# Kernel optimization log

Measured on AMD Instinct MI355X. Metric: run time of the kernel, lower is better.

## Reference

```python
import jax, jax.numpy as jnp
import numpy as np

N, E, F_IN, HID, EDIM = 20000, 320000, 16, 64, 1


def _add_self_loops(src, dst, eattr, n):
    # PyG add_self_loops with fill_value='mean': self-loop edge_attr = mean of
    # incoming edge_attr per destination node (0 if no incoming edges).
    deg = jax.ops.segment_sum(jnp.ones_like(eattr[:, 0]), dst, num_segments=n)
    mean_attr = jax.ops.segment_sum(eattr, dst, num_segments=n) / jnp.maximum(deg, 1.0)[:, None]
    loop = jnp.arange(n)
    return (jnp.concatenate([src, loop]), jnp.concatenate([dst, loop]),
            jnp.concatenate([eattr, mean_attr], axis=0))


def _gat_layer(x, src, dst, eattr, W, a_src, a_dst, We, a_e, b, heads, out_ch, n):
    # shared linear for src/dst (PyG GATConv with int in_channels)
    h = (x @ W).reshape(n, heads, out_ch)                      # [N,H,C]
    al_s = jnp.einsum('nhc,hc->nh', h, a_src)                  # [N,H]
    al_d = jnp.einsum('nhc,hc->nh', h, a_dst)
    ef = (eattr @ We).reshape(-1, heads, out_ch)               # [E,H,C]
    al_e = jnp.einsum('ehc,hc->eh', ef, a_e)                   # [E,H]
    alpha = jax.nn.leaky_relu(al_s[src] + al_d[dst] + al_e, 0.2)
    # segment softmax over destination node
    m = jax.ops.segment_max(alpha, dst, num_segments=n)
    m = jnp.where(jnp.isfinite(m), m, 0.0)
    ex = jnp.exp(alpha - m[dst])
    den = jax.ops.segment_sum(ex, dst, num_segments=n)
    coef = ex / (den[dst] + 1e-16)                             # [E,H]
    out = jax.ops.segment_sum(h[src] * coef[:, :, None], dst, num_segments=n)
    return out.reshape(n, heads * out_ch) + b


def setup_inputs() -> dict:
    key = jax.random.key(0)
    ks = jax.random.split(key, 24)
    s = 0.1
    inp = {
        'x': jax.random.normal(ks[0], (N, F_IN), jnp.float32),
        'edge_index': jax.random.randint(ks[1], (2, E), 0, N, jnp.int64),
        'edge_attr': jax.random.uniform(ks[2], (E, EDIM), jnp.float32),
        # layer 0: heads=4, in=16, out=64
        'W0': jax.random.normal(ks[3], (F_IN, 4 * HID), jnp.float32) * s,
        'as0': jax.random.normal(ks[4], (4, HID), jnp.float32) * s,
        'ad0': jax.random.normal(ks[5], (4, HID), jnp.float32) * s,
        'We0': jax.random.normal(ks[6], (EDIM, 4 * HID), jnp.float32) * s,
        'ae0': jax.random.normal(ks[7], (4, HID), jnp.float32) * s,
        'b0': jnp.zeros((4 * HID,), jnp.float32),
        # layer 1: heads=4, in=256, out=64
        'W1': jax.random.normal(ks[8], (4 * HID, 4 * HID), jnp.float32) * s,
        'as1': jax.random.normal(ks[9], (4, HID), jnp.float32) * s,
        'ad1': jax.random.normal(ks[10], (4, HID), jnp.float32) * s,
        'We1': jax.random.normal(ks[11], (EDIM, 4 * HID), jnp.float32) * s,
        'ae1': jax.random.normal(ks[12], (4, HID), jnp.float32) * s,
        'b1': jnp.zeros((4 * HID,), jnp.float32),
        # layer 2: heads=1, in=256, out=64
        'W2': jax.random.normal(ks[13], (4 * HID, HID), jnp.float32) * s,
        'as2': jax.random.normal(ks[14], (1, HID), jnp.float32) * s,
        'ad2': jax.random.normal(ks[15], (1, HID), jnp.float32) * s,
        'We2': jax.random.normal(ks[16], (EDIM, HID), jnp.float32) * s,
        'ae2': jax.random.normal(ks[17], (1, HID), jnp.float32) * s,
        'b2': jnp.zeros((HID,), jnp.float32),
        'ln_g': jnp.ones((HID,), jnp.float32),
        'ln_b': jnp.zeros((HID,), jnp.float32),
    }
    return inp


def reference(x, edge_index, edge_attr,
              W0, as0, ad0, We0, ae0, b0,
              W1, as1, ad1, We1, ae1, b1,
              W2, as2, ad2, We2, ae2, b2,
              ln_g, ln_b):
    n = x.shape[0]
    src, dst, eattr = _add_self_loops(edge_index[0], edge_index[1], edge_attr, n)
    h = _gat_layer(x, src, dst, eattr, W0, as0, ad0, We0, ae0, b0, 4, HID, n)
    h = jax.nn.elu(h)  # dropout is identity in eval
    h = _gat_layer(h, src, dst, eattr, W1, as1, ad1, We1, ae1, b1, 4, HID, n)
    h = jax.nn.elu(h)
    h = _gat_layer(h, src, dst, eattr, W2, as2, ad2, We2, ae2, b2, 1, HID, n)
    mu = jnp.mean(h, axis=-1, keepdims=True)
    var = jnp.mean((h - mu) ** 2, axis=-1, keepdims=True)
    return (h - mu) / jnp.sqrt(var + 1e-5) * ln_g + ln_b
```

## Files before the change

kernel.cpp:

```cpp
#include <hip/hip_runtime.h>
#include <hip/hip_bf16.h>
#include <math.h>


typedef __attribute__((ext_vector_type(8))) short short8;
typedef __attribute__((ext_vector_type(4))) float float4v;

#define CAP 64

__device__ __forceinline__ float wave_sum(float v) {
#pragma unroll
  for (int off = 32; off > 0; off >>= 1) v += __shfl_xor(v, off, 64);
  return v;
}

__device__ __forceinline__ unsigned short f2bf(float v) {
  unsigned u = __float_as_uint(v);
  unsigned r = u + 0x7fff + ((u >> 16) & 1);
  return (unsigned short)(r >> 16);
}

__device__ __forceinline__ float bf2f(unsigned short u) {
  return __uint_as_float(((unsigned)u) << 16);
}

__global__ __launch_bounds__(256) void k1_kernel(
    const float* __restrict__ x, const int* __restrict__ srcv, const int* __restrict__ dstv,
    const float* __restrict__ eattr,
    const float* __restrict__ W0, const float* __restrict__ as0, const float* __restrict__ ad0,
    const float* __restrict__ We0, const float* __restrict__ ae0,
    const float* __restrict__ W1, const float* __restrict__ as1, const float* __restrict__ ad1,
    const float* __restrict__ We1, const float* __restrict__ ae1,
    const float* __restrict__ W2, const float* __restrict__ as2, const float* __restrict__ ad2,
    const float* __restrict__ We2, const float* __restrict__ ae2,
    unsigned short* __restrict__ Wf1, unsigned short* __restrict__ Wf2,
    float* __restrict__ wedot, float* __restrict__ al0s, float* __restrict__ al0d,
    int* __restrict__ deg, int2* __restrict__ ebuf,
    int N, int E, int gD) {
  int b = blockIdx.x;
  int tid = threadIdx.x;
  if (b < 272) {
    int idx = b * 256 + tid;
    int j = idx & 7, lane = (idx >> 3) & 63, ks = (idx >> 9) & 7, nt = idx >> 12;
    int k = ks * 32 + (lane >> 4) * 8 + j;
    int col = lane & 15;
    float v = 0.f;
    if (nt < 16) {
      v = W1[(size_t)k * 256 + nt * 16 + col];
    } else if (col < 4) {
      for (int c = 0; c < 64; c++) v = fmaf(W1[(size_t)k * 256 + col * 64 + c], as1[col * 64 + c], v);
    } else if (col < 8) {
      int h = col - 4;
      for (int c = 0; c < 64; c++) v = fmaf(W1[(size_t)k * 256 + h * 64 + c], ad1[h * 64 + c], v);
    }
    Wf1[idx] = f2bf(v);
  } else if (b < 352) {
    int idx = (b - 272) * 256 + tid;
    int j = idx & 7, lane = (idx >> 3) & 63, ks = (idx >> 9) & 7, nt = idx >> 12;
    int k = ks * 32 + (lane >> 4) * 8 + j;
    int col = lane & 15;
    float v = 0.f;
    if (nt < 4) {
      v = W2[(size_t)k * 64 + nt * 16 + col];
    } else if (col < 1) {
      for (int c = 0; c < 64; c++) v = fmaf(W2[(size_t)k * 64 + c], as2[c], v);
    } else if (col < 2) {
      for (int c = 0; c < 64; c++) v = fmaf(W2[(size_t)k * 64 + c], ad2[c], v);
    }
    Wf2[idx] = f2bf(v);
  } else if (b == 352) {
    if (tid >= 64) return;
    int c = tid;
    for (int h = 0; h < 4; h++) {
      float v = wave_sum(We0[h * 64 + c] * ae0[h * 64 + c]);
      if (c == 0) wedot[h] = v;
    }
    for (int h = 0; h < 4; h++) {
      float v = wave_sum(We1[h * 64 + c] * ae1[h * 64 + c]);
      if (c == 0) wedot[4 + h] = v;
    }
    float v = wave_sum(We2[c] * ae2[c]);
    if (c == 0) wedot[8] = v;
  } else if (b < 353 + gD) {
    __shared__ float va[128];
    if (tid < 128) {
      int k = tid >> 3, col = tid & 7;
      float v = 0.f;
      if (col < 4) {
        for (int c = 0; c < 64; c++) v = fmaf(W0[(size_t)k * 256 + col * 64 + c], as0[col * 64 + c], v);
      } else {
        int h = col - 4;
        for (int c = 0; c < 64; c++) v = fmaf(W0[(size_t)k * 256 + h * 64 + c], ad0[h * 64 + c], v);
      }
      va[tid] = v;
    }
    __syncthreads();
    int node = (b - 353) * 256 + tid;
    if (node >= N) return;
    const float4* xr = (const float4*)(x + (size_t)node * 16);
    float4 xv[4];
#pragma unroll
    for (int q = 0; q < 4; q++) xv[q] = xr[q];
    float al[8];
#pragma unroll
    for (int j = 0; j < 8; j++) al[j] = 0.f;
#pragma unroll
    for (int k = 0; k < 16; k++) {
      float xk = ((const float*)xv)[k];
#pragma unroll
      for (int j = 0; j < 8; j++) al[j] = fmaf(xk, va[k * 8 + j], al[j]);
    }
    ((float4*)al0s)[node] = make_float4(al[0], al[1], al[2], al[3]);
    ((float4*)al0d)[node] = make_float4(al[4], al[5], al[6], al[7]);
  } else {
    int e = (b - 353 - gD) * 256 + tid;
    if (e >= E) return;
    int d = dstv[e];
    int s = srcv[e];
    float ea = eattr[e];
    int pos = atomicAdd(&deg[d], 1);
    if (pos < CAP) ebuf[(size_t)d * CAP + pos] = make_int2(s, __float_as_int(ea));
  }
}

__global__ __launch_bounds__(256) void fused0_kernel(
    const int* __restrict__ deg, const int2* __restrict__ ebuf,
    const float* __restrict__ al0s, const float* __restrict__ al0d,
    const float* __restrict__ wedot,
    const float* __restrict__ x, const float* __restrict__ W0,
    const float* __restrict__ b0, const unsigned short* __restrict__ Wf1,
    unsigned short* __restrict__ buf256, float* __restrict__ al1s,
    float* __restrict__ al1d, int n) {
  __shared__ unsigned short hrow[16][264];
  int tile = blockIdx.x;
  int wv = threadIdx.x >> 6;
  int lane = threadIdx.x & 63;
  int es = lane >> 4;
  int c = lane & 15;

  for (int s = 0; s < 4; s++) {
    int r = wv * 4 + s;
    int node = tile * 16 + r;
    if (node < n) {
      int dg = deg[node];
      int cnt = dg < CAP ? dg : CAP;
      float xself = x[(size_t)node * 16 + c];
      float4 as4s = ((const float4*)al0s)[node];
      float4 ald = ((const float4*)al0d)[node];
      float wd[4];
#pragma unroll
      for (int h = 0; h < 4; h++) wd[h] = wedot[h];

      float Z[4] = {0.f, 0.f, 0.f, 0.f};
      float den[4] = {0.f, 0.f, 0.f, 0.f};
      float easum = 0.f;

      for (int i = 0; i < cnt; i += 4) {
        int base = __builtin_amdgcn_readfirstlane(node * CAP + i);
        int2 r0 = ebuf[base], r1 = ebuf[base + 1], r2 = ebuf[base + 2], r3 = ebuf[base + 3];
        int2 rm = (es == 0) ? r0 : (es == 1) ? r1 : (es == 2) ? r2 : r3;
        bool valid = (i + es) < cnt;
        int src = valid ? rm.x : 0;
        float ev = valid ? __int_as_float(rm.y) : 0.f;
        float xv = x[(size_t)src * 16 + c];
        float4 as4 = ((const float4*)al0s)[src];
        easum += ev;
#pragma unroll
        for (int h = 0; h < 4; h++) {
          float a = ((const float*)&as4)[h] + ((const float*)&ald)[h] + ev * wd[h];
          a = fmaxf(a, 0.2f * a);
          a = fminf(a, 30.f);
          float wvv = __expf(a);
          wvv = valid ? wvv : 0.f;
          den[h] += wvv;
          Z[h] = fmaf(wvv, xv, Z[h]);
        }
      }

#pragma unroll
      for (int h = 0; h < 4; h++) {
        Z[h] += __shfl_xor(Z[h], 16, 64);
        Z[h] += __shfl_xor(Z[h], 32, 64);
        den[h] += __shfl_xor(den[h], 16, 64);
        den[h] += __shfl_xor(den[h], 32, 64);
      }
      easum += __shfl_xor(easum, 16, 64);
      easum += __shfl_xor(easum, 32, 64);

      {
        float evs = easum / fmaxf((float)dg, 1.f);
#pragma unroll
        for (int h = 0; h < 4; h++) {
          float a = ((const float*)&as4s)[h] + ((const float*)&ald)[h] + evs * wd[h];
          a = fmaxf(a, 0.2f * a);
          a = fminf(a, 30.f);
          float wvv = __expf(a);
          den[h] += wvv;
          Z[h] = fmaf(wvv, xself, Z[h]);
        }
      }

      int h = es;
      float zsel = (h == 0) ? Z[0] : (h == 1) ? Z[1] : (h == 2) ? Z[2] : Z[3];
      float dsel = (h == 0) ? den[0] : (h == 1) ? den[1] : (h == 2) ? den[2] : den[3];
      float zn = zsel / (dsel + 1e-16f);
      float4 w0r[16];
#pragma unroll
      for (int cc = 0; cc < 16; cc++) w0r[cc] = ((const float4*)(W0 + (size_t)cc * 256))[lane];
      float zc[16];
      int basel = lane & 48;
#pragma unroll
      for (int cc = 0; cc < 16; cc++) zc[cc] = __shfl(zn, basel + cc, 64);
      float o[4];
      float4 b4 = ((const float4*)b0)[lane];
#pragma unroll
      for (int jj = 0; jj < 4; jj++) o[jj] = ((const float*)&b4)[jj];
#pragma unroll
      for (int cc = 0; cc < 16; cc++) {
#pragma unroll
        for (int jj = 0; jj < 4; jj++) o[jj] = fmaf(zc[cc], ((const float*)&w0r[cc])[jj], o[jj]);
      }
      ushort4 o4;
      float ox = o[0] > 0.f ? o[0] : expm1f(o[0]);
      float oy = o[1] > 0.f ? o[1] : expm1f(o[1]);
      float oz = o[2] > 0.f ? o[2] : expm1f(o[2]);
      float ow = o[3] > 0.f ? o[3] : expm1f(o[3]);
      o4.x = f2bf(ox);
      o4.y = f2bf(oy);
      o4.z = f2bf(oz);
      o4.w = f2bf(ow);
      *(ushort4*)&hrow[r][lane * 4] = o4;
    } else {
      *(ushort4*)&hrow[r][lane * 4] = make_ushort4(0, 0, 0, 0);
    }
  }
  __syncthreads();

  int m = lane & 15, q = lane >> 4;
  int row0 = tile * 16;
  short8 afrag[8];
#pragma unroll
  for (int ks = 0; ks < 8; ks++) afrag[ks] = *(short8*)&hrow[m][ks * 32 + q * 8];

  const short8* wf = (const short8*)Wf1;
  for (int nt = wv; nt < 17; nt += 4) {
    const short8* bl = wf + (size_t)nt * 8 * 64 + lane;
    short8 bf[8];
#pragma unroll
    for (int ks = 0; ks < 8; ks++) bf[ks] = bl[ks * 64];
    float4v acc = {0.f, 0.f, 0.f, 0.f};
#pragma unroll
    for (int ks = 0; ks < 8; ks++)
      acc = __builtin_amdgcn_mfma_f32_16x16x32_bf16(afrag[ks], bf[ks], acc, 0, 0, 0);
    if (nt < 16) {
      int col = nt * 16 + m;
#pragma unroll
      for (int reg = 0; reg < 4; reg++) {
        int rr = row0 + q * 4 + reg;
        if (rr < n) buf256[(size_t)rr * 256 + col] = f2bf(acc[reg]);
      }
    } else {
#pragma unroll
      for (int reg = 0; reg < 4; reg++) {
        int rr = row0 + q * 4 + reg;
        if (rr < n) {
          if (m < 4) al1s[(size_t)rr * 4 + m] = acc[reg];
          else if (m < 8) al1d[(size_t)rr * 4 + (m - 4)] = acc[reg];
        }
      }
    }
  }
}

__global__ __launch_bounds__(256) void fused1_kernel(
    const int* __restrict__ deg, const int2* __restrict__ ebuf,
    const float* __restrict__ al1s, const float* __restrict__ al1d,
    const float* __restrict__ wedot,
    const unsigned short* __restrict__ buf256, const float* __restrict__ b1,
    const unsigned short* __restrict__ Wf2, unsigned short* __restrict__ buf64,
    float* __restrict__ al2s, float* __restrict__ al2d, int n) {
  __shared__ unsigned short hrow[16][264];
  int tile = blockIdx.x;
  int wv = threadIdx.x >> 6;
  int lane = threadIdx.x & 63;
  int half = lane >> 5;
  int l = lane & 31;
  int h4 = l >> 3;

  for (int s = 0; s < 4; s++) {
    int r = wv * 4 + s;
    int node = tile * 16 + r;
    if (node < n) {
      int dg = deg[node];
      int cnt = dg < CAP ? dg : CAP;
      float aldh = al1d[(size_t)node * 4 + h4];
      float alsh = al1s[(size_t)node * 4 + h4];
      float wdh = wedot[4 + h4];
      short8 rowS = ((const short8*)(buf256 + (size_t)node * 256))[l];

      float acc[8];
#pragma unroll
      for (int j = 0; j < 8; j++) acc[j] = 0.f;
      float den = 0.f;
      float easum = 0.f;

      for (int i = 0; i < cnt; i += 4) {
        int base = __builtin_amdgcn_readfirstlane(node * CAP + i);
        int2 r0 = ebuf[base], r1 = ebuf[base + 1], r2 = ebuf[base + 2], r3 = ebuf[base + 3];
        bool vA = (i + (half ? 1 : 0)) < cnt;
        bool vB = (i + (half ? 3 : 2)) < cnt;
        int2 rA = half ? r1 : r0;
        int2 rB = half ? r3 : r2;
        int srcA = vA ? rA.x : 0;
        int srcB = vB ? rB.x : 0;
        float evA = vA ? __int_as_float(rA.y) : 0.f;
        float evB = vB ? __int_as_float(rB.y) : 0.f;
        easum += evA + evB;
        float aA = al1s[(size_t)srcA * 4 + h4] + aldh + evA * wdh;
        float aB = al1s[(size_t)srcB * 4 + h4] + aldh + evB * wdh;
        aA = fmaxf(aA, 0.2f * aA);
        aB = fmaxf(aB, 0.2f * aB);
        aA = fminf(aA, 30.f);
        aB = fminf(aB, 30.f);
        float wA = __expf(aA);
        float wB = __expf(aB);
        wA = vA ? wA : 0.f;
        wB = vB ? wB : 0.f;
        short8 rowA = ((const short8*)(buf256 + (size_t)srcA * 256))[l];
        short8 rowB = ((const short8*)(buf256 + (size_t)srcB * 256))[l];
        den += wA + wB;
        const unsigned short* pa = (const unsigned short*)&rowA;
        const unsigned short* pb = (const unsigned short*)&rowB;
#pragma unroll
        for (int j = 0; j < 8; j++) acc[j] = fmaf(wA, bf2f(pa[j]), acc[j]);
#pragma unroll
        for (int j = 0; j < 8; j++) acc[j] = fmaf(wB, bf2f(pb[j]), acc[j]);
      }

      den += __shfl_xor(den, 32, 64);
      easum += __shfl_xor(easum, 32, 64);
#pragma unroll
      for (int j = 0; j < 8; j++) acc[j] += __shfl_xor(acc[j], 32, 64);

      {
        float evs = easum / fmaxf((float)dg, 1.f);
        float a = alsh + aldh + evs * wdh;
        a = fmaxf(a, 0.2f * a);
        a = fminf(a, 30.f);
        float wvv = __expf(a);
        const unsigned short* ps = (const unsigned short*)&rowS;
        den += wvv;
#pragma unroll
        for (int j = 0; j < 8; j++) acc[j] = fmaf(wvv, bf2f(ps[j]), acc[j]);
      }

      if (half == 0) {
        float inv = 1.f / (den + 1e-16f);
        float4 bb0 = ((const float4*)b1)[l * 2];
        float4 bb1 = ((const float4*)b1)[l * 2 + 1];
        unsigned short o8[8];
#pragma unroll
        for (int j = 0; j < 8; j++) {
          float bjv = (j < 4) ? ((const float*)&bb0)[j] : ((const float*)&bb1)[j - 4];
          float o = acc[j] * inv + bjv;
          o = o > 0.f ? o : expm1f(o);
          o8[j] = f2bf(o);
        }
        *(short8*)&hrow[r][l * 8] = *(short8*)o8;
      }
    } else if (half == 0) {
      unsigned short z8[8] = {0, 0, 0, 0, 0, 0, 0, 0};
      *(short8*)&hrow[r][l * 8] = *(short8*)z8;
    }
  }
  __syncthreads();

  int m = lane & 15, q = lane >> 4;
  int row0 = tile * 16;
  short8 afrag[8];
#pragma unroll
  for (int ks = 0; ks < 8; ks++) afrag[ks] = *(short8*)&hrow[m][ks * 32 + q * 8];

  const short8* wf = (const short8*)Wf2;
  for (int nt = wv; nt < 5; nt += 4) {
    const short8* bl = wf + (size_t)nt * 8 * 64 + lane;
    short8 bf[8];
#pragma unroll
    for (int ks = 0; ks < 8; ks++) bf[ks] = bl[ks * 64];
    float4v acc = {0.f, 0.f, 0.f, 0.f};
#pragma unroll
    for (int ks = 0; ks < 8; ks++)
      acc = __builtin_amdgcn_mfma_f32_16x16x32_bf16(afrag[ks], bf[ks], acc, 0, 0, 0);
    if (nt < 4) {
      int col = nt * 16 + m;
#pragma unroll
      for (int reg = 0; reg < 4; reg++) {
        int rr = row0 + q * 4 + reg;
        if (rr < n) buf64[(size_t)rr * 64 + col] = f2bf(acc[reg]);
      }
    } else {
#pragma unroll
      for (int reg = 0; reg < 4; reg++) {
        int rr = row0 + q * 4 + reg;
        if (rr < n) {
          if (m < 1) al2s[rr] = acc[reg];
          else if (m < 2) al2d[rr] = acc[reg];
        }
      }
    }
  }
}

__global__ __launch_bounds__(256) void agg_ln_kernel(
    const int* __restrict__ deg, const int2* __restrict__ ebuf,
    const float* __restrict__ al2s, const float* __restrict__ al2d,
    const float* __restrict__ wedot,
    const unsigned short* __restrict__ B, const float* __restrict__ bias,
    const float* __restrict__ ln_g, const float* __restrict__ ln_b,
    float* __restrict__ out, int n) {
  int node = blockIdx.x * 4 + (threadIdx.x >> 6);
  if (node >= n) return;
  int lane = threadIdx.x & 63;
  int q = lane >> 4;
  int l = lane & 15;
  int dg = deg[node];
  int cnt = dg < CAP ? dg : CAP;
  float ald = al2d[node];
  float als = al2s[node];
  float wd = wedot[0];
  ushort4 bvS = ((const ushort4*)(B + (size_t)node * 64))[l];

  float4 acc = make_float4(0.f, 0.f, 0.f, 0.f);
  float den = 0.f;
  float easum = 0.f;

  for (int i = 0; i < cnt; i += 4) {
    int base = __builtin_amdgcn_readfirstlane(node * CAP + i);
    int2 r0 = ebuf[base], r1 = ebuf[base + 1], r2 = ebuf[base + 2], r3 = ebuf[base + 3];
    int2 rm = (q == 0) ? r0 : (q == 1) ? r1 : (q == 2) ? r2 : r3;
    bool valid = (i + q) < cnt;
    int src = valid ? rm.x : 0;
    float ev = valid ? __int_as_float(rm.y) : 0.f;
    easum += ev;
    float a = al2s[src] + ald + ev * wd;
    a = fmaxf(a, 0.2f * a);
    a = fminf(a, 30.f);
    float wv = __expf(a);
    wv = valid ? wv : 0.f;
    ushort4 bv = ((const ushort4*)(B + (size_t)src * 64))[l];
    den += wv;
    acc.x = fmaf(wv, bf2f(bv.x), acc.x);
    acc.y = fmaf(wv, bf2f(bv.y), acc.y);
    acc.z = fmaf(wv, bf2f(bv.z), acc.z);
    acc.w = fmaf(wv, bf2f(bv.w), acc.w);
  }

  den += __shfl_xor(den, 32, 64);
  den += __shfl_xor(den, 16, 64);
  easum += __shfl_xor(easum, 32, 64);
  easum += __shfl_xor(easum, 16, 64);
  acc.x += __shfl_xor(acc.x, 32, 64);
  acc.y += __shfl_xor(acc.y, 32, 64);
  acc.z += __shfl_xor(acc.z, 32, 64);
  acc.w += __shfl_xor(acc.w, 32, 64);
  acc.x += __shfl_xor(acc.x, 16, 64);
  acc.y += __shfl_xor(acc.y, 16, 64);
  acc.z += __shfl_xor(acc.z, 16, 64);
  acc.w += __shfl_xor(acc.w, 16, 64);

  {
    float evs = easum / fmaxf((float)dg, 1.f);
    float a = als + ald + evs * wd;
    a = fmaxf(a, 0.2f * a);
    a = fminf(a, 30.f);
    float wv = __expf(a);
    den += wv;
    acc.x = fmaf(wv, bf2f(bvS.x), acc.x);
    acc.y = fmaf(wv, bf2f(bvS.y), acc.y);
    acc.z = fmaf(wv, bf2f(bvS.z), acc.z);
    acc.w = fmaf(wv, bf2f(bvS.w), acc.w);
  }

  float inv = 1.f / (den + 1e-16f);
  float4 b4 = ((const float4*)bias)[l];
  float4 o;
  o.x = acc.x * inv + b4.x;
  o.y = acc.y * inv + b4.y;
  o.z = acc.z * inv + b4.z;
  o.w = acc.w * inv + b4.w;
  float s = (o.x + o.y) + (o.z + o.w);
#pragma unroll
  for (int off = 1; off < 16; off <<= 1) s += __shfl_xor(s, off, 64);
  float mu = s * (1.f / 64.f);
  float dx = o.x - mu, dy = o.y - mu, dz = o.z - mu, dw = o.w - mu;
  float v = (dx * dx + dy * dy) + (dz * dz + dw * dw);
#pragma unroll
  for (int off = 1; off < 16; off <<= 1) v += __shfl_xor(v, off, 64);
  float rs = rsqrtf(v * (1.f / 64.f) + 1e-5f);
  if (q == 0) {
    float4 g4 = ((const float4*)ln_g)[l];
    float4 lb4 = ((const float4*)ln_b)[l];
    float4 rr;
    rr.x = dx * rs * g4.x + lb4.x;
    rr.y = dy * rs * g4.y + lb4.y;
    rr.z = dz * rs * g4.z + lb4.z;
    rr.w = dw * rs * g4.w + lb4.w;
    ((float4*)(out + (size_t)node * 64))[l] = rr;
  }
}

extern "C" void kernel_launch(void* const* d_in, const int* in_sizes, int n_in,
                              void* d_out, int out_size, void* d_ws, size_t ws_size,
                              hipStream_t stream) {
  const float* x = (const float*)d_in[0];
  const int* ei = (const int*)d_in[1];
  const float* eattr = (const float*)d_in[2];
  const float* W0 = (const float*)d_in[3];
  const float* as0 = (const float*)d_in[4];
  const float* ad0 = (const float*)d_in[5];
  const float* We0 = (const float*)d_in[6];
  const float* ae0 = (const float*)d_in[7];
  const float* b0 = (const float*)d_in[8];
  const float* W1 = (const float*)d_in[9];
  const float* as1 = (const float*)d_in[10];
  const float* ad1 = (const float*)d_in[11];
  const float* We1 = (const float*)d_in[12];
  const float* ae1 = (const float*)d_in[13];
  const float* b1 = (const float*)d_in[14];
  const float* W2 = (const float*)d_in[15];
  const float* as2 = (const float*)d_in[16];
  const float* ad2 = (const float*)d_in[17];
  const float* We2 = (const float*)d_in[18];
  const float* ae2 = (const float*)d_in[19];
  const float* b2 = (const float*)d_in[20];
  const float* lng = (const float*)d_in[21];
  const float* lnb = (const float*)d_in[22];
  float* outp = (float*)d_out;

  const int N = in_sizes[0] / 16;
  const int E = in_sizes[1] / 2;
  const int* srcv = ei;
  const int* dstv = ei + E;

  char* w = (char*)d_ws;
  size_t off = 0;
  auto alloc = [&](size_t bytes) -> void* {
    void* p = w + off;
    off += (bytes + 255) & ~(size_t)255;
    return p;
  };
  int* deg = (int*)alloc((size_t)N * 4);
  size_t zero_bytes = off;
  int2* ebuf = (int2*)alloc(((size_t)N * CAP + 8) * 8);
  float* wedot = (float*)alloc(16 * 4);
  float* al0s = (float*)alloc((size_t)N * 4 * 4);
  float* al0d = (float*)alloc((size_t)N * 4 * 4);
  float* al1s = (float*)alloc((size_t)N * 4 * 4);
  float* al1d = (float*)alloc((size_t)N * 4 * 4);
  float* al2s = (float*)alloc((size_t)N * 4);
  float* al2d = (float*)alloc((size_t)N * 4);
  unsigned short* Wf1 = (unsigned short*)alloc((size_t)17 * 4096 * 2);
  unsigned short* Wf2 = (unsigned short*)alloc((size_t)5 * 4096 * 2);
  unsigned short* buf256 = (unsigned short*)alloc((size_t)N * 256 * 2);
  unsigned short* buf64 = (unsigned short*)alloc((size_t)N * 64 * 2);
  (void)ws_size;

  hipMemsetAsync(d_ws, 0, zero_bytes, stream);

  int gE = (E + 255) / 256;
  int gD = (N + 255) / 256;

  k1_kernel<<<353 + gD + gE, 256, 0, stream>>>(
      x, srcv, dstv, eattr, W0, as0, ad0, We0, ae0, W1, as1, ad1, We1, ae1,
      W2, as2, ad2, We2, ae2, Wf1, Wf2, wedot, al0s, al0d, deg, ebuf, N, E, gD);

  int gT = (N + 15) / 16;
  int gNode4 = (N + 3) / 4;

  fused0_kernel<<<gT, 256, 0, stream>>>(deg, ebuf, al0s, al0d, wedot, x, W0, b0,
                                        Wf1, buf256, al1s, al1d, N);

  fused1_kernel<<<gT, 256, 0, stream>>>(deg, ebuf, al1s, al1d, wedot, buf256, b1,
                                        Wf2, buf64, al2s, al2d, N);

  agg_ln_kernel<<<gNode4, 256, 0, stream>>>(deg, ebuf, al2s, al2d, wedot + 8,
                                            buf64, b2, lng, lnb, outp, N);
}
```

Before: 214.6 us.

## Compute edge attention weights once per edge-head and share via LDS

The edge loops in the three aggregation kernels are restructured. Each wave now loads 16 edge records at once, with one lane per edge-head pair. Each lane computes that pair's leaky-relu and exp a single time and writes the weight and source index into per-wave LDS. Lanes then read these staged values back to gather neighbour features. Before, every lane recomputed all four heads' exps for its edge and pulled edge records through scalar broadcast loads. The aim is to cut this redundant transcendental work and load overhead. The cost is extra LDS traffic and a reliance on wave-local LDS ordering with no barrier.

```diff
diff --git a/kernel.cpp b/kernel.cpp
--- a/kernel.cpp
+++ b/kernel.cpp
@@ -22,6 +22,10 @@
 
 __device__ __forceinline__ float bf2f(unsigned short u) {
   return __uint_as_float(((unsigned)u) << 16);
+}
+
+__device__ __forceinline__ float sel4(float a, float b, float c, float d, int i) {
+  return (i == 0) ? a : (i == 1) ? b : (i == 2) ? c : d;
 }
 
 __global__ __launch_bounds__(256) void k1_kernel(
@@ -132,11 +136,15 @@
     unsigned short* __restrict__ buf256, float* __restrict__ al1s,
     float* __restrict__ al1d, int n) {
   __shared__ unsigned short hrow[16][264];
+  __shared__ __align__(16) float wbuf[4][16][4];
+  __shared__ int sbuf[4][16];
   int tile = blockIdx.x;
   int wv = threadIdx.x >> 6;
   int lane = threadIdx.x & 63;
   int es = lane >> 4;
   int c = lane & 15;
+  int le = lane >> 2;
+  int lh = lane & 3;
 
   for (int s = 0; s < 4; s++) {
     int r = wv * 4 + s;
@@ -146,34 +154,40 @@
       int cnt = dg < CAP ? dg : CAP;
       float xself = x[(size_t)node * 16 + c];
       float4 as4s = ((const float4*)al0s)[node];
-      float4 ald = ((const float4*)al0d)[node];
-      float wd[4];
-#pragma unroll
-      for (int h = 0; h < 4; h++) wd[h] = wedot[h];
+      float4 ald4 = ((const float4*)al0d)[node];
+      float aldP = ((const float*)&ald4)[0];
+      aldP = sel4(ald4.x, ald4.y, ald4.z, ald4.w, lh);
+      float wd0 = wedot[0], wd1 = wedot[1], wd2 = wedot[2], wd3 = wedot[3];
+      float wdP = sel4(wd0, wd1, wd2, wd3, lh);
 
       float Z[4] = {0.f, 0.f, 0.f, 0.f};
-      float den[4] = {0.f, 0.f, 0.f, 0.f};
-      float easum = 0.f;
-
-      for (int i = 0; i < cnt; i += 4) {
-        int base = __builtin_amdgcn_readfirstlane(node * CAP + i);
-        int2 r0 = ebuf[base], r1 = ebuf[base + 1], r2 = ebuf[base + 2], r3 = ebuf[base + 3];
-        int2 rm = (es == 0) ? r0 : (es == 1) ? r1 : (es == 2) ? r2 : r3;
-        bool valid = (i + es) < cnt;
-        int src = valid ? rm.x : 0;
-        float ev = valid ? __int_as_float(rm.y) : 0.f;
-        float xv = x[(size_t)src * 16 + c];
-        float4 as4 = ((const float4*)al0s)[src];
-        easum += ev;
-#pragma unroll
-        for (int h = 0; h < 4; h++) {
-          float a = ((const float*)&as4)[h] + ((const float*)&ald)[h] + ev * wd[h];
-          a = fmaxf(a, 0.2f * a);
-          a = fminf(a, 30.f);
-          float wvv = __expf(a);
-          wvv = valid ? wvv : 0.f;
-          den[h] += wvv;
-          Z[h] = fmaf(wvv, xv, Z[h]);
+      float denP = 0.f;
+      float easumP = 0.f;
+
+      for (int i = 0; i < cnt; i += 16) {
+        int slot = i + le;
+        bool av = slot < cnt;
+        int2 re = ebuf[(size_t)node * CAP + slot];
+        int srcE = av ? re.x : 0;
+        float ev = av ? __int_as_float(re.y) : 0.f;
+        float a = al0s[(size_t)srcE * 4 + lh] + aldP + ev * wdP;
+        a = fmaxf(a, 0.2f * a);
+        a = fminf(a, 30.f);
+        float wE = av ? __expf(a) : 0.f;
+        denP += wE;
+        easumP += (lh == 0) ? ev : 0.f;
+        wbuf[wv][le][lh] = wE;
+        if (lh == 0) sbuf[wv][le] = srcE;
+#pragma unroll
+        for (int k = 0; k < 4; k++) {
+          int e = k * 4 + es;
+          float4 w4 = *(const float4*)&wbuf[wv][e][0];
+          int srcX = sbuf[wv][e];
+          float xv = x[(size_t)srcX * 16 + c];
+          Z[0] = fmaf(w4.x, xv, Z[0]);
+          Z[1] = fmaf(w4.y, xv, Z[1]);
+          Z[2] = fmaf(w4.z, xv, Z[2]);
+          Z[3] = fmaf(w4.w, xv, Z[3]);
         }
       }
 
@@ -181,29 +195,26 @@
       for (int h = 0; h < 4; h++) {
         Z[h] += __shfl_xor(Z[h], 16, 64);
         Z[h] += __shfl_xor(Z[h], 32, 64);
-        den[h] += __shfl_xor(den[h], 16, 64);
-        den[h] += __shfl_xor(den[h], 32, 64);
-      }
-      easum += __shfl_xor(easum, 16, 64);
-      easum += __shfl_xor(easum, 32, 64);
-
-      {
-        float evs = easum / fmaxf((float)dg, 1.f);
-#pragma unroll
-        for (int h = 0; h < 4; h++) {
-          float a = ((const float*)&as4s)[h] + ((const float*)&ald)[h] + evs * wd[h];
-          a = fmaxf(a, 0.2f * a);
-          a = fminf(a, 30.f);
-          float wvv = __expf(a);
-          den[h] += wvv;
-          Z[h] = fmaf(wvv, xself, Z[h]);
-        }
-      }
-
-      int h = es;
-      float zsel = (h == 0) ? Z[0] : (h == 1) ? Z[1] : (h == 2) ? Z[2] : Z[3];
-      float dsel = (h == 0) ? den[0] : (h == 1) ? den[1] : (h == 2) ? den[2] : den[3];
+      }
+      denP += __shfl_xor(denP, 4, 64);
+      denP += __shfl_xor(denP, 8, 64);
+      denP += __shfl_xor(denP, 16, 64);
+      denP += __shfl_xor(denP, 32, 64);
+      float easum = wave_sum(easumP);
+
+      float dsel = __shfl(denP, es, 64);
+      float evs = easum / fmaxf((float)dg, 1.f);
+      float as_e = sel4(as4s.x, as4s.y, as4s.z, as4s.w, es);
+      float ald_e = sel4(ald4.x, ald4.y, ald4.z, ald4.w, es);
+      float wd_e = sel4(wd0, wd1, wd2, wd3, es);
+      float aS = as_e + ald_e + evs * wd_e;
+      aS = fmaxf(aS, 0.2f * aS);
+      aS = fminf(aS, 30.f);
+      float wvs = __expf(aS);
+      dsel += wvs;
+      float zsel = sel4(Z[0], Z[1], Z[2], Z[3], es) + wvs * xself;
       float zn = zsel / (dsel + 1e-16f);
+
       float4 w0r[16];
 #pragma unroll
       for (int cc = 0; cc < 16; cc++) w0r[cc] = ((const float4*)(W0 + (size_t)cc * 256))[lane];
@@ -280,12 +291,16 @@
     const unsigned short* __restrict__ Wf2, unsigned short* __restrict__ buf64,
     float* __restrict__ al2s, float* __restrict__ al2d, int n) {
   __shared__ unsigned short hrow[16][264];
+  __shared__ __align__(16) float wbuf[4][16][4];
+  __shared__ int sbuf[4][16];
   int tile = blockIdx.x;
   int wv = threadIdx.x >> 6;
   int lane = threadIdx.x & 63;
   int half = lane >> 5;
   int l = lane & 31;
   int h4 = l >> 3;
+  int le = lane >> 2;
+  int lh = lane & 3;
 
   for (int s = 0; s < 4; s++) {
     int r = wv * 4 + s;
@@ -296,51 +311,57 @@
       float aldh = al1d[(size_t)node * 4 + h4];
       float alsh = al1s[(size_t)node * 4 + h4];
       float wdh = wedot[4 + h4];
+      float aldP = al1d[(size_t)node * 4 + lh];
+      float wdP = wedot[4 + lh];
       short8 rowS = ((const short8*)(buf256 + (size_t)node * 256))[l];
 
       float acc[8];
 #pragma unroll
       for (int j = 0; j < 8; j++) acc[j] = 0.f;
-      float den = 0.f;
-      float easum = 0.f;
-
-      for (int i = 0; i < cnt; i += 4) {
-        int base = __builtin_amdgcn_readfirstlane(node * CAP + i);
-        int2 r0 = ebuf[base], r1 = ebuf[base + 1], r2 = ebuf[base + 2], r3 = ebuf[base + 3];
-        bool vA = (i + (half ? 1 : 0)) < cnt;
-        bool vB = (i + (half ? 3 : 2)) < cnt;
-        int2 rA = half ? r1 : r0;
-        int2 rB = half ? r3 : r2;
-        int srcA = vA ? rA.x : 0;
-        int srcB = vB ? rB.x : 0;
-        float evA = vA ? __int_as_float(rA.y) : 0.f;
-        float evB = vB ? __int_as_float(rB.y) : 0.f;
-        easum += evA + evB;
-        float aA = al1s[(size_t)srcA * 4 + h4] + aldh + evA * wdh;
-        float aB = al1s[(size_t)srcB * 4 + h4] + aldh + evB * wdh;
-        aA = fmaxf(aA, 0.2f * aA);
-        aB = fmaxf(aB, 0.2f * aB);
-        aA = fminf(aA, 30.f);
-        aB = fminf(aB, 30.f);
-        float wA = __expf(aA);
-        float wB = __expf(aB);
-        wA = vA ? wA : 0.f;
-        wB = vB ? wB : 0.f;
-        short8 rowA = ((const short8*)(buf256 + (size_t)srcA * 256))[l];
-        short8 rowB = ((const short8*)(buf256 + (size_t)srcB * 256))[l];
-        den += wA + wB;
-        const unsigned short* pa = (const unsigned short*)&rowA;
-        const unsigned short* pb = (const unsigned short*)&rowB;
-#pragma unroll
-        for (int j = 0; j < 8; j++) acc[j] = fmaf(wA, bf2f(pa[j]), acc[j]);
-#pragma unroll
-        for (int j = 0; j < 8; j++) acc[j] = fmaf(wB, bf2f(pb[j]), acc[j]);
-      }
-
-      den += __shfl_xor(den, 32, 64);
-      easum += __shfl_xor(easum, 32, 64);
+      float denP = 0.f;
+      float easumP = 0.f;
+
+      for (int i = 0; i < cnt; i += 16) {
+        int slot = i + le;
+        bool av = slot < cnt;
+        int2 re = ebuf[(size_t)node * CAP + slot];
+        int srcE = av ? re.x : 0;
+        float ev = av ? __int_as_float(re.y) : 0.f;
+        float a = al1s[(size_t)srcE * 4 + lh] + aldP + ev * wdP;
+        a = fmaxf(a, 0.2f * a);
+        a = fminf(a, 30.f);
+        float wE = av ? __expf(a) : 0.f;
+        denP += wE;
+        easumP += (lh == 0) ? ev : 0.f;
+        wbuf[wv][le][lh] = wE;
+        if (lh == 0) sbuf[wv][le] = srcE;
+#pragma unroll
+        for (int k = 0; k < 4; k++) {
+          int eA = k * 4 + (half ? 1 : 0);
+          int eB = k * 4 + (half ? 3 : 2);
+          float wA = wbuf[wv][eA][h4];
+          float wB = wbuf[wv][eB][h4];
+          int srcA = sbuf[wv][eA];
+          int srcB = sbuf[wv][eB];
+          short8 rowA = ((const short8*)(buf256 + (size_t)srcA * 256))[l];
+          short8 rowB = ((const short8*)(buf256 + (size_t)srcB * 256))[l];
+          const unsigned short* pa = (const unsigned short*)&rowA;
+          const unsigned short* pb = (const unsigned short*)&rowB;
+#pragma unroll
+          for (int j = 0; j < 8; j++) acc[j] = fmaf(wA, bf2f(pa[j]), acc[j]);
+#pragma unroll
+          for (int j = 0; j < 8; j++) acc[j] = fmaf(wB, bf2f(pb[j]), acc[j]);
+        }
+      }
+
 #pragma unroll
       for (int j = 0; j < 8; j++) acc[j] += __shfl_xor(acc[j], 32, 64);
+      denP += __shfl_xor(denP, 4, 64);
+      denP += __shfl_xor(denP, 8, 64);
+      denP += __shfl_xor(denP, 16, 64);
+      denP += __shfl_xor(denP, 32, 64);
+      float easum = wave_sum(easumP);
+      float den = __shfl(denP, h4, 64);
 
       {
         float evs = easum / fmaxf((float)dg, 1.f);
@@ -368,9 +389,9 @@
         }
         *(short8*)&hrow[r][l * 8] = *(short8*)o8;
       }
-    } else if (half == 0) {
+    } else if ((lane >> 5) == 0) {
       unsigned short z8[8] = {0, 0, 0, 0, 0, 0, 0, 0};
-      *(short8*)&hrow[r][l * 8] = *(short8*)z8;
+      *(short8*)&hrow[r][(lane & 31) * 8] = *(short8*)z8;
     }
   }
   __syncthreads();
@@ -418,11 +439,15 @@
     const unsigned short* __restrict__ B, const float* __restrict__ bias,
     const float* __restrict__ ln_g, const float* __restrict__ ln_b,
     float* __restrict__ out, int n) {
-  int node = blockIdx.x * 4 + (threadIdx.x >> 6);
+  __shared__ float wbuf[4][16];
+  __shared__ int sbuf[4][16];
+  int wv = threadIdx.x >> 6;
+  int node = blockIdx.x * 4 + wv;
   if (node >= n) return;
   int lane = threadIdx.x & 63;
   int q = lane >> 4;
   int l = lane & 15;
+  int le = lane & 15;
   int dg = deg[node];
   int cnt = dg < CAP ? dg : CAP;
   float ald = al2d[node];
@@ -431,34 +456,38 @@
   ushort4 bvS = ((const ushort4*)(B + (size_t)node * 64))[l];
 
   float4 acc = make_float4(0.f, 0.f, 0.f, 0.f);
-  float den = 0.f;
-  float easum = 0.f;
-
-  for (int i = 0; i < cnt; i += 4) {
-    int base = __builtin_amdgcn_readfirstlane(node * CAP + i);
-    int2 r0 = ebuf[base], r1 = ebuf[base + 1], r2 = ebuf[base + 2], r3 = ebuf[base + 3];
-    int2 rm = (q == 0) ? r0 : (q == 1) ? r1 : (q == 2) ? r2 : r3;
-    bool valid = (i + q) < cnt;
-    int src = valid ? rm.x : 0;
-    float ev = valid ? __int_as_float(rm.y) : 0.f;
-    easum += ev;
-    float a = al2s[src] + ald + ev * wd;
+  float denP = 0.f;
+  float easumP = 0.f;
+
+  for (int i = 0; i < cnt; i += 16) {
+    int slot = i + le;
+    bool av = slot < cnt;
+    int2 re = ebuf[(size_t)node * CAP + slot];
+    int srcE = av ? re.x : 0;
+    float ev = av ? __int_as_float(re.y) : 0.f;
+    float a = al2s[srcE] + ald + ev * wd;
     a = fmaxf(a, 0.2f * a);
     a = fminf(a, 30.f);
-    float wv = __expf(a);
-    wv = valid ? wv : 0.f;
-    ushort4 bv = ((const ushort4*)(B + (size_t)src * 64))[l];
-    den += wv;
-    acc.x = fmaf(wv, bf2f(bv.x), acc.x);
-    acc.y = fmaf(wv, bf2f(bv.y), acc.y);
-    acc.z = fmaf(wv, bf2f(bv.z), acc.z);
-    acc.w = fmaf(wv, bf2f(bv.w), acc.w);
-  }
-
-  den += __shfl_xor(den, 32, 64);
-  den += __shfl_xor(den, 16, 64);
-  easum += __shfl_xor(easum, 32, 64);
-  easum += __shfl_xor(easum, 16, 64);
+    float wE = av ? __expf(a) : 0.f;
+    denP += wE;
+    easumP += ev;
+    if (lane < 16) {
+      wbuf[wv][le] = wE;
+      sbuf[wv][le] = srcE;
+    }
+#pragma unroll
+    for (int k = 0; k < 4; k++) {
+      int e = k * 4 + q;
+      float w = wbuf[wv][e];
+      int src = sbuf[wv][e];
+      ushort4 bv = ((const ushort4*)(B + (size_t)src * 64))[l];
+      acc.x = fmaf(w, bf2f(bv.x), acc.x);
+      acc.y = fmaf(w, bf2f(bv.y), acc.y);
+      acc.z = fmaf(w, bf2f(bv.z), acc.z);
+      acc.w = fmaf(w, bf2f(bv.w), acc.w);
+    }
+  }
+
   acc.x += __shfl_xor(acc.x, 32, 64);
   acc.y += __shfl_xor(acc.y, 32, 64);
   acc.z += __shfl_xor(acc.z, 32, 64);
@@ -467,18 +496,20 @@
   acc.y += __shfl_xor(acc.y, 16, 64);
   acc.z += __shfl_xor(acc.z, 16, 64);
   acc.w += __shfl_xor(acc.w, 16, 64);
+  float den = wave_sum(denP) * 0.25f;
+  float easum = wave_sum(easumP) * 0.25f;
 
   {
     float evs = easum / fmaxf((float)dg, 1.f);
     float a = als + ald + evs * wd;
     a = fmaxf(a, 0.2f * a);
     a = fminf(a, 30.f);
-    float wv = __expf(a);
-    den += wv;
-    acc.x = fmaf(wv, bf2f(bvS.x), acc.x);
-    acc.y = fmaf(wv, bf2f(bvS.y), acc.y);
-    acc.z = fmaf(wv, bf2f(bvS.z), acc.z);
-    acc.w = fmaf(wv, bf2f(bvS.w), acc.w);
+    float wv2 = __expf(a);
+    den += wv2;
+    acc.x = fmaf(wv2, bf2f(bvS.x), acc.x);
+    acc.y = fmaf(wv2, bf2f(bvS.y), acc.y);
+    acc.z = fmaf(wv2, bf2f(bvS.z), acc.z);
+    acc.w = fmaf(wv2, bf2f(bvS.w), acc.w);
   }
 
   float inv = 1.f / (den + 1e-16f);
@@ -551,7 +582,7 @@
   };
   int* deg = (int*)alloc((size_t)N * 4);
   size_t zero_bytes = off;
-  int2* ebuf = (int2*)alloc(((size_t)N * CAP + 8) * 8);
+  int2* ebuf = (int2*)alloc(((size_t)N * CAP + 16) * 8);
   float* wedot = (float*)alloc(16 * 4);
   float* al0s = (float*)alloc((size_t)N * 4 * 4);
   float* al0d = (float*)alloc((size_t)N * 4 * 4);
```

Result: no change. 215.7 us (+0.5%).
